# Kernel optimization log

Hardware: AMD Instinct MI355X
Metric: run time of the kernel (lower is better)

## Reference

```python
import jax, jax.numpy as jnp
import numpy as np

NEG_SLOPE = 0.2  # PyG GATConv default LeakyReLU slope
EPS = 1e-16


def gat_conv(x, src, dst, W, att_src, att_dst, bias, concat):
    """One GATConv layer (PyG semantics, self-loops already in src/dst).
    x: [N, Fin]; src/dst: [E'] int; W: [Fin, H*C]; att_*: [H, C]; bias: [H*C] or [C].
    """
    N = x.shape[0]
    H, C = att_src.shape
    h = (x @ W).reshape(N, H, C)                      # [N, H, C]
    a_s = jnp.einsum('nhc,hc->nh', h, att_src)        # [N, H]
    a_d = jnp.einsum('nhc,hc->nh', h, att_dst)        # [N, H]
    logits = jax.nn.leaky_relu(a_s[src] + a_d[dst], NEG_SLOPE)  # [E', H]
    # segment softmax over incoming edges of each destination node
    m = jax.ops.segment_max(logits, dst, num_segments=N)        # [N, H]
    m = jnp.where(jnp.isfinite(m), m, 0.0)
    e = jnp.exp(logits - m[dst])                                # [E', H]
    denom = jax.ops.segment_sum(e, dst, num_segments=N)         # [N, H]
    alpha = e / (denom[dst] + EPS)                              # [E', H]
    msg = h[src] * alpha[:, :, None]                            # [E', H, C]
    out = jax.ops.segment_sum(msg, dst, num_segments=N)         # [N, H, C]
    out = out.reshape(N, H * C) if concat else out.mean(axis=1)
    return out + bias


def setup_inputs() -> dict:
    key = jax.random.key(0)
    ks = jax.random.split(key, 8)
    N, E, IN, HID, OUT, H1 = 50000, 800000, 128, 64, 32, 2
    x = jax.random.normal(ks[0], (N, IN), dtype=jnp.float32)
    edge_index = jax.random.randint(ks[1], (2, E), 0, N, dtype=jnp.int32)
    # glorot-ish scaled params
    W1 = jax.random.normal(ks[2], (IN, H1 * HID), dtype=jnp.float32) * (1.0 / np.sqrt(IN))
    att_src1 = jax.random.normal(ks[3], (H1, HID), dtype=jnp.float32) * (1.0 / np.sqrt(HID))
    att_dst1 = jax.random.normal(ks[4], (H1, HID), dtype=jnp.float32) * (1.0 / np.sqrt(HID))
    bias1 = jnp.zeros((H1 * HID,), dtype=jnp.float32)
    W2 = jax.random.normal(ks[5], (H1 * HID, OUT), dtype=jnp.float32) * (1.0 / np.sqrt(H1 * HID))
    att_src2 = jax.random.normal(ks[6], (1, OUT), dtype=jnp.float32) * (1.0 / np.sqrt(OUT))
    att_dst2 = jax.random.normal(ks[7], (1, OUT), dtype=jnp.float32) * (1.0 / np.sqrt(OUT))
    bias2 = jnp.zeros((OUT,), dtype=jnp.float32)
    return {"x": x, "edge_index": edge_index, "W1": W1, "att_src1": att_src1,
            "att_dst1": att_dst1, "bias1": bias1, "W2": W2, "att_src2": att_src2,
            "att_dst2": att_dst2, "bias2": bias2}


def reference(x, edge_index, W1, att_src1, att_dst1, bias1, W2, att_src2, att_dst2, bias2):
    N = x.shape[0]
    loops = jnp.arange(N, dtype=edge_index.dtype)
    src = jnp.concatenate([edge_index[0], loops])   # add self loops (PyG default)
    dst = jnp.concatenate([edge_index[1], loops])
    h = gat_conv(x, src, dst, W1, att_src1, att_dst1, bias1, concat=True)
    h = jax.nn.relu(h)
    out = gat_conv(h, src, dst, W2, att_src2, att_dst2, bias2, concat=False)
    return out
```

## Files before the change

### kernel.cpp

```cpp
#include <hip/hip_runtime.h>
#include <math.h>


typedef __bf16 bf16x8 __attribute__((ext_vector_type(8)));
typedef float f32x4 __attribute__((ext_vector_type(4)));

__device__ __forceinline__ float lrelu(float x) { return x > 0.f ? x : 0.2f * x; }

__device__ __forceinline__ unsigned short f2bf(float x) {
  unsigned u = __float_as_uint(x);
  return (unsigned short)((u + 0x7fffu + ((u >> 16) & 1u)) >> 16);
}
__device__ __forceinline__ float2 bf2_unpack(unsigned u) {
  return make_float2(__uint_as_float(u << 16), __uint_as_float(u & 0xffff0000u));
}

constexpr int CAP2 = 1408;

union SharedK1 {
  struct { int hist[1024]; int bbase[1024]; } part;
  union { unsigned short bl[32 * 64 * 8]; float accl[64 * 132]; } gem;
};

__launch_bounds__(256)
__global__ void k_csr_gemm1(const int* __restrict__ srcA, const int* __restrict__ dstA,
                            int E, int Nn, int PB, int* __restrict__ gcnt,
                            unsigned* __restrict__ bkt,
                            const float* __restrict__ A, const float* __restrict__ B,
                            unsigned short* __restrict__ Cb,
                            const float* __restrict__ attS, const float* __restrict__ attD,
                            float* __restrict__ asO, float* __restrict__ adO, int M) {
  __shared__ SharedK1 sm;
  const int tid = threadIdx.x;
  if ((int)blockIdx.x < PB) {
    const int NBK = (Nn + 63) >> 6;
    for (int i = tid; i < NBK; i += 256) sm.part.hist[i] = 0;
    __syncthreads();
    const int tot = E + Nn;
    const int g0 = blockIdx.x * 4096;
    unsigned pk[16]; int bk[16], rk[16]; int cnt = 0;
#pragma unroll
    for (int j = 0; j < 16; ++j) {
      int g = g0 + j * 256 + tid;
      if (g >= tot) break;
      int s, d;
      if (g < E) { s = srcA[g]; d = dstA[g]; } else { s = g - E; d = s; }
      int b = d >> 6;
      pk[cnt] = (unsigned)s | ((unsigned)(d & 63) << 16);
      bk[cnt] = b;
      rk[cnt] = atomicAdd(&sm.part.hist[b], 1);
      cnt++;
    }
    __syncthreads();
    for (int i = tid; i < NBK; i += 256) {
      int h = sm.part.hist[i];
      sm.part.bbase[i] = h ? atomicAdd(&gcnt[i], h) : 0;
    }
    __syncthreads();
    for (int j = 0; j < cnt; ++j) {
      int pos = sm.part.bbase[bk[j]] + rk[j];
      if (pos < CAP2) bkt[(size_t)bk[j] * CAP2 + pos] = pk[j];
    }
    return;
  }
  const int lane = tid & 63, w = tid >> 6;
  const int row0 = (blockIdx.x - PB) * 64;
  for (int i = tid; i < 128 * 32; i += 256) {
    int k = i >> 5, n4 = (i & 31) << 2;
    float4 v = *(const float4*)(B + k * 128 + n4);
    int c = k >> 5, q = (k >> 3) & 3, j = k & 7;
    float vv[4] = {v.x, v.y, v.z, v.w};
#pragma unroll
    for (int u2 = 0; u2 < 4; ++u2) {
      int n = n4 + u2, t = n >> 4, l = q * 16 + (n & 15);
      sm.gem.bl[((t * 4 + c) * 64 + l) * 8 + j] = f2bf(vv[u2]);
    }
  }
  int mrow = row0 + 16 * w + (lane & 15);
  bool rok = mrow < M;
  const int q = lane >> 4;
  bf16x8 afr[4];
  union { unsigned short s[8]; bf16x8 b; } cv;
#pragma unroll
  for (int c = 0; c < 4; ++c) {
    float4 u0 = make_float4(0.f, 0.f, 0.f, 0.f), u1 = u0;
    if (rok) {
      const float* ap = A + (size_t)mrow * 128 + c * 32 + q * 8;
      u0 = *(const float4*)ap; u1 = *(const float4*)(ap + 4);
    }
    cv.s[0] = f2bf(u0.x); cv.s[1] = f2bf(u0.y); cv.s[2] = f2bf(u0.z); cv.s[3] = f2bf(u0.w);
    cv.s[4] = f2bf(u1.x); cv.s[5] = f2bf(u1.y); cv.s[6] = f2bf(u1.z); cv.s[7] = f2bf(u1.w);
    afr[c] = cv.b;
  }
  __syncthreads();
  f32x4 acc[8];
#pragma unroll
  for (int t = 0; t < 8; ++t) {
    f32x4 a = {0.f, 0.f, 0.f, 0.f};
#pragma unroll
    for (int c = 0; c < 4; ++c) {
      bf16x8 bf = *(((const bf16x8*)sm.gem.bl) + (t * 4 + c) * 64 + lane);
      a = __builtin_amdgcn_mfma_f32_16x16x32_bf16(afr[c], bf, a, 0, 0, 0);
    }
    acc[t] = a;
  }
  __syncthreads();
  {
    int rbase = 16 * w + q * 4, cl = lane & 15;
#pragma unroll
    for (int t = 0; t < 8; ++t)
#pragma unroll
      for (int r = 0; r < 4; ++r)
        sm.gem.accl[(rbase + r) * 132 + 16 * t + cl] = acc[t][r];
  }
  __syncthreads();
  {
    int row = tid >> 2, cg = tid & 3, c0 = cg * 32;
    int grow = row0 + row;
    const float* ar = &sm.gem.accl[row * 132 + c0];
    float ps = 0.f, pd = 0.f;
    unsigned pkv[16];
#pragma unroll
    for (int u2 = 0; u2 < 8; ++u2) {
      float4 v  = *(const float4*)(ar + u2 * 4);
      float4 s4 = *(const float4*)(attS + c0 + u2 * 4);
      float4 d4 = *(const float4*)(attD + c0 + u2 * 4);
      ps += v.x * s4.x + v.y * s4.y + v.z * s4.z + v.w * s4.w;
      pd += v.x * d4.x + v.y * d4.y + v.z * d4.z + v.w * d4.w;
      pkv[u2 * 2]     = (unsigned)f2bf(v.x) | ((unsigned)f2bf(v.y) << 16);
      pkv[u2 * 2 + 1] = (unsigned)f2bf(v.z) | ((unsigned)f2bf(v.w) << 16);
    }
    ps += __shfl_xor(ps, 1); pd += __shfl_xor(pd, 1);
    if (grow < M) {
      if ((tid & 1) == 0) {
        int head = (tid >> 1) & 1;
        asO[(size_t)grow * 2 + head] = ps; adO[(size_t)grow * 2 + head] = pd;
      }
      unsigned* cp = (unsigned*)(Cb + (size_t)grow * 128 + c0);
      *(uint4*)(cp)      = make_uint4(pkv[0], pkv[1], pkv[2], pkv[3]);
      *(uint4*)(cp + 4)  = make_uint4(pkv[4], pkv[5], pkv[6], pkv[7]);
      *(uint4*)(cp + 8)  = make_uint4(pkv[8], pkv[9], pkv[10], pkv[11]);
      *(uint4*)(cp + 12) = make_uint4(pkv[12], pkv[13], pkv[14], pkv[15]);
    }
  }
}

__launch_bounds__(512)
__global__ void k_fused2(const unsigned* __restrict__ bkt, const int* __restrict__ gcnt,
                         int Nn, int tot,
                         const float* __restrict__ as1, const float* __restrict__ ad1,
                         const float* __restrict__ bias1,
                         const unsigned* __restrict__ h1b,
                         const float* __restrict__ W2,
                         const float* __restrict__ attS, const float* __restrict__ attD,
                         int* __restrict__ offs, unsigned short* __restrict__ csr16,
                         unsigned short* __restrict__ h2b,
                         float* __restrict__ as2, float* __restrict__ ad2) {
  __shared__ unsigned short bl[8 * 64 * 8];
  __shared__ unsigned h2t[64 * 68];
  __shared__ unsigned short srcL[CAP2];
  __shared__ int fc[64], lo[65], cur[64];
  __shared__ float accl[64 * 36];
  __shared__ int baseS;
  const int b = blockIdx.x;
  const int tid = threadIdx.x;
  int m = gcnt[b]; if (m > CAP2) m = CAP2;
  const unsigned* p = bkt + (size_t)b * CAP2;

  for (int i = tid; i < 128 * 8; i += 512) {
    int k = i >> 3, n4 = (i & 7) << 2;
    float4 v = *(const float4*)(W2 + k * 32 + n4);
    int c = k >> 5, q = (k >> 3) & 3, j = k & 7;
    float vv[4] = {v.x, v.y, v.z, v.w};
#pragma unroll
    for (int u2 = 0; u2 < 4; ++u2) {
      int n = n4 + u2, t = n >> 4, l = q * 16 + (n & 15);
      bl[((t * 4 + c) * 64 + l) * 8 + j] = f2bf(vv[u2]);
    }
  }
  if (tid < 64) fc[tid] = 0;
  if (b == 0 && tid == 64) offs[Nn] = tot;
  __syncthreads();
  for (int i = tid; i < m; i += 512) atomicAdd(&fc[p[i] >> 16], 1);
  __syncthreads();
  if (tid < 64) {
    int s = 0;
    for (int c = tid; c < b; c += 64) s += gcnt[c];
#pragma unroll
    for (int o = 32; o; o >>= 1) s += __shfl_xor(s, o);
    if (tid == 0) baseS = s;
    int v = fc[tid], x = v;
#pragma unroll
    for (int o = 1; o < 64; o <<= 1) { int t = __shfl_up(x, o); if (tid >= o) x += t; }
    lo[tid] = x - v;
    cur[tid] = x - v;
    if (tid == 63) lo[64] = x;
  }
  __syncthreads();
  for (int i = tid; i < m; i += 512) {
    unsigned e = p[i];
    int pos = atomicAdd(&cur[e >> 16], 1);
    srcL[pos] = (unsigned short)(e & 0xffffu);
  }
  __syncthreads();
  const int base = baseS;
  for (int i = tid; i < m; i += 512) csr16[base + i] = srcL[i];
  if (tid < 64) {
    int n = (b << 6) + tid;
    if (n < Nn) offs[n] = base + lo[tid];
  }

  const int w = tid >> 6, lane = tid & 63;
  const int head = lane >> 5, el = lane & 31;
  const int pbase = (lane & 32) << 2;
  for (int j8 = 0; j8 < 8; ++j8) {
    int j = w * 8 + j8;
    int n = (b << 6) + j;
    if (n >= Nn) break;
    int beg = lo[j], end = lo[j + 1];
    float2 adn = ((const float2*)ad1)[n];
    float adh = head ? adn.y : adn.x;
    float ax = 0.f, ay = 0.f, den = 0.f;
    int i = beg;
    while (i < end) {
      int mm = end - i; if (mm > 32) mm = 32;
      bool ok = el < mm;
      int sv = ok ? (int)srcL[i + el] : 0;
      float wv = 0.f;
      if (ok) {
        float2 a = ((const float2*)as1)[sv];
        wv = __expf(lrelu((head ? a.y : a.x) + adh));
      }
      int j2 = 0;
      for (; j2 + 4 <= mm; j2 += 4) {
#pragma unroll
        for (int u = 0; u < 4; ++u) {
          int s = __builtin_amdgcn_readlane(sv, j2 + u);
          float ee = __int_as_float(
              __builtin_amdgcn_ds_bpermute(pbase + 4 * (j2 + u), __float_as_int(wv)));
          float2 v = bf2_unpack(h1b[(size_t)s * 64 + lane]);
          ax += ee * v.x; ay += ee * v.y; den += ee;
        }
      }
      for (; j2 < mm; ++j2) {
        int s = __builtin_amdgcn_readlane(sv, j2);
        float ee = __int_as_float(
            __builtin_amdgcn_ds_bpermute(pbase + 4 * j2, __float_as_int(wv)));
        float2 v = bf2_unpack(h1b[(size_t)s * 64 + lane]);
        ax += ee * v.x; ay += ee * v.y; den += ee;
      }
      i += mm;
    }
    float inv = 1.f / (den + 1e-16f);
    const float2 bv = ((const float2*)bias1)[lane];
    float o0 = ax * inv + bv.x; o0 = o0 > 0.f ? o0 : 0.f;
    float o1 = ay * inv + bv.y; o1 = o1 > 0.f ? o1 : 0.f;
    h2t[j * 68 + lane] = (unsigned)f2bf(o0) | ((unsigned)f2bf(o1) << 16);
  }
  __syncthreads();

  {
    int rt = w & 3, ct = w >> 2;
    int mloc = rt * 16 + (lane & 15);
    int q = lane >> 4;
    bf16x8 afr[4];
#pragma unroll
    for (int c = 0; c < 4; ++c) {
      uint4 u = *(const uint4*)&h2t[mloc * 68 + c * 16 + q * 4];
      afr[c] = __builtin_bit_cast(bf16x8, u);
    }
    f32x4 a = {0.f, 0.f, 0.f, 0.f};
#pragma unroll
    for (int c = 0; c < 4; ++c) {
      bf16x8 bf = *(((const bf16x8*)bl) + (ct * 4 + c) * 64 + lane);
      a = __builtin_amdgcn_mfma_f32_16x16x32_bf16(afr[c], bf, a, 0, 0, 0);
    }
    int rbase = rt * 16 + q * 4, cl = lane & 15;
#pragma unroll
    for (int r = 0; r < 4; ++r)
      accl[(rbase + r) * 36 + ct * 16 + cl] = a[r];
  }
  __syncthreads();
  if (tid < 256) {
    int row = tid >> 2, cg = tid & 3, c0 = cg * 8;
    int grow = (b << 6) + row;
    const float* ar = &accl[row * 36 + c0];
    float ps = 0.f, pd = 0.f;
    unsigned pkv[4];
#pragma unroll
    for (int u2 = 0; u2 < 2; ++u2) {
      float4 v  = *(const float4*)(ar + u2 * 4);
      float4 s4 = *(const float4*)(attS + c0 + u2 * 4);
      float4 d4 = *(const float4*)(attD + c0 + u2 * 4);
      ps += v.x * s4.x + v.y * s4.y + v.z * s4.z + v.w * s4.w;
      pd += v.x * d4.x + v.y * d4.y + v.z * d4.z + v.w * d4.w;
      pkv[u2 * 2]     = (unsigned)f2bf(v.x) | ((unsigned)f2bf(v.y) << 16);
      pkv[u2 * 2 + 1] = (unsigned)f2bf(v.z) | ((unsigned)f2bf(v.w) << 16);
    }
    ps += __shfl_xor(ps, 1); ps += __shfl_xor(ps, 2);
    pd += __shfl_xor(pd, 1); pd += __shfl_xor(pd, 2);
    if (grow < Nn) {
      if (cg == 0) { as2[grow] = ps; ad2[grow] = pd; }
      *(uint4*)(h2b + (size_t)grow * 32 + c0) = make_uint4(pkv[0], pkv[1], pkv[2], pkv[3]);
    }
  }
}

__global__ void k_agg2(const unsigned* __restrict__ h2b, const float* __restrict__ as2,
                       const float* __restrict__ ad2, const int* __restrict__ offs,
                       const unsigned short* __restrict__ csr16,
                       const float* __restrict__ bias, float* __restrict__ out, int Nn) {
  int n = blockIdx.x * (blockDim.x >> 6) + (threadIdx.x >> 6);
  if (n >= Nn) return;
  int lane = threadIdx.x & 63;
  int g = lane >> 4, cp = lane & 15;
  int beg = offs[n], end = offs[n + 1];
  float adn = ad2[n];
  float ax = 0.f, ay = 0.f, den = 0.f;
  int i = beg;
  while (i < end) {
    int m = end - i; if (m > 64) m = 64;
    int idx = i + lane;
    bool ok = idx < end;
    int sv = ok ? (int)csr16[idx] : 0;
    float wv = ok ? __expf(lrelu(as2[sv] + adn)) : 0.f;
    for (int j = 0; j < m; j += 4) {
      int jj = j + g;
      float ee = __shfl(wv, jj);
      int s = __shfl(sv, jj);
      float2 v = bf2_unpack(h2b[(size_t)s * 16 + cp]);
      ax += ee * v.x; ay += ee * v.y; den += ee;
    }
    i += m;
  }
  ax += __shfl_xor(ax, 16); ay += __shfl_xor(ay, 16); den += __shfl_xor(den, 16);
  ax += __shfl_xor(ax, 32); ay += __shfl_xor(ay, 32); den += __shfl_xor(den, 32);
  if (lane < 16) {
    float inv = 1.f / (den + 1e-16f);
    const float2 bv = ((const float2*)bias)[cp];
    ((float2*)out)[(size_t)n * 16 + cp] =
        make_float2(ax * inv + bv.x, ay * inv + bv.y);
  }
}

extern "C" void kernel_launch(void* const* d_in, const int* in_sizes, int n_in,
                              void* d_out, int out_size, void* d_ws, size_t ws_size,
                              hipStream_t stream) {
  const float* x      = (const float*)d_in[0];
  const int*   ei     = (const int*)d_in[1];
  const float* W1     = (const float*)d_in[2];
  const float* att_s1 = (const float*)d_in[3];
  const float* att_d1 = (const float*)d_in[4];
  const float* bias1  = (const float*)d_in[5];
  const float* W2     = (const float*)d_in[6];
  const float* att_s2 = (const float*)d_in[7];
  const float* att_d2 = (const float*)d_in[8];
  const float* bias2  = (const float*)d_in[9];
  float* out = (float*)d_out;

  const int N = in_sizes[0] / 128;
  const int E = in_sizes[1] / 2;
  const int* srcA = ei;
  const int* dstA = ei + E;
  const int tot = E + N;
  const int NBK = (N + 63) >> 6;

  char* w = (char*)d_ws;
  auto alloc = [&](size_t bytes) { char* p = w; w += (bytes + 255) / 256 * 256; return p; };
  unsigned short* h1b = (unsigned short*)alloc((size_t)N * 128 * 2);
  unsigned short* h2b = (unsigned short*)alloc((size_t)N * 32 * 2);
  float* as1    = (float*)alloc((size_t)N * 2 * 4);
  float* ad1    = (float*)alloc((size_t)N * 2 * 4);
  float* as2    = (float*)alloc((size_t)N * 4);
  float* ad2    = (float*)alloc((size_t)N * 4);
  int*   gcnt   = (int*)alloc((size_t)NBK * 4);
  unsigned* bkt = (unsigned*)alloc((size_t)NBK * CAP2 * 4);
  int*   offs   = (int*)alloc((size_t)(N + 1) * 4);
  unsigned short* csr16 = (unsigned short*)alloc((size_t)tot * 2);

  hipMemsetAsync(gcnt, 0, (size_t)NBK * 4, stream);

  const int PB = (tot + 4095) / 4096;
  const int GB = (N + 63) / 64;
  k_csr_gemm1<<<PB + GB, 256, 0, stream>>>(srcA, dstA, E, N, PB, gcnt, bkt,
                                           x, W1, h1b, att_s1, att_d1, as1, ad1, N);
  k_fused2<<<NBK, 512, 0, stream>>>(bkt, gcnt, N, tot, as1, ad1, bias1,
                                    (const unsigned*)h1b, W2, att_s2, att_d2,
                                    offs, csr16, h2b, as2, ad2);
  int nb = (N + 3) / 4;
  k_agg2<<<nb, 256, 0, stream>>>((const unsigned*)h2b, as2, ad2, offs, csr16, bias2, out, N);
}
```

Measured before the change: 181.9 us.

## Merge layer-2 aggregation into fused kernel via global spin barrier

k_fused2 now makes each block handle two 64-node buckets, then waits at a grid-wide atomic spin barrier before running the layer-2 aggregation that used to be the separate k_agg2 launch. This removes one kernel launch and its tail gap, and amortises the W2 shared-memory staging over two buckets. The barrier only works if all 391 blocks are resident at once, which launch_bounds(512,4) is meant to help ensure. If they are not co-resident it deadlocks, and halving the block count reduces parallelism in the aggregation phases.

```diff
diff --git a/kernel.cpp b/kernel.cpp
--- a/kernel.cpp
+++ b/kernel.cpp
@@ -145,9 +145,9 @@
   }
 }
 
-__launch_bounds__(512)
+__launch_bounds__(512, 4)
 __global__ void k_fused2(const unsigned* __restrict__ bkt, const int* __restrict__ gcnt,
-                         int Nn, int tot,
+                         int Nn, int tot, int NBK,
                          const float* __restrict__ as1, const float* __restrict__ ad1,
                          const float* __restrict__ bias1,
                          const unsigned* __restrict__ h1b,
@@ -155,17 +155,17 @@
                          const float* __restrict__ attS, const float* __restrict__ attD,
                          int* __restrict__ offs, unsigned short* __restrict__ csr16,
                          unsigned short* __restrict__ h2b,
-                         float* __restrict__ as2, float* __restrict__ ad2) {
+                         float* __restrict__ as2, float* __restrict__ ad2,
+                         const float* __restrict__ bias2, float* __restrict__ out,
+                         unsigned* __restrict__ barrier_ctr) {
   __shared__ unsigned short bl[8 * 64 * 8];
   __shared__ unsigned h2t[64 * 68];
   __shared__ unsigned short srcL[CAP2];
   __shared__ int fc[64], lo[65], cur[64];
   __shared__ float accl[64 * 36];
   __shared__ int baseS;
-  const int b = blockIdx.x;
   const int tid = threadIdx.x;
-  int m = gcnt[b]; if (m > CAP2) m = CAP2;
-  const unsigned* p = bkt + (size_t)b * CAP2;
+  const int w = tid >> 6, lane = tid & 63;
 
   for (int i = tid; i < 128 * 8; i += 512) {
     int k = i >> 3, n4 = (i & 7) << 2;
@@ -178,168 +178,183 @@
       bl[((t * 4 + c) * 64 + l) * 8 + j] = f2bf(vv[u2]);
     }
   }
-  if (tid < 64) fc[tid] = 0;
-  if (b == 0 && tid == 64) offs[Nn] = tot;
-  __syncthreads();
-  for (int i = tid; i < m; i += 512) atomicAdd(&fc[p[i] >> 16], 1);
-  __syncthreads();
-  if (tid < 64) {
-    int s = 0;
-    for (int c = tid; c < b; c += 64) s += gcnt[c];
-#pragma unroll
-    for (int o = 32; o; o >>= 1) s += __shfl_xor(s, o);
-    if (tid == 0) baseS = s;
-    int v = fc[tid], x = v;
-#pragma unroll
-    for (int o = 1; o < 64; o <<= 1) { int t = __shfl_up(x, o); if (tid >= o) x += t; }
-    lo[tid] = x - v;
-    cur[tid] = x - v;
-    if (tid == 63) lo[64] = x;
-  }
-  __syncthreads();
-  for (int i = tid; i < m; i += 512) {
-    unsigned e = p[i];
-    int pos = atomicAdd(&cur[e >> 16], 1);
-    srcL[pos] = (unsigned short)(e & 0xffffu);
-  }
-  __syncthreads();
-  const int base = baseS;
-  for (int i = tid; i < m; i += 512) csr16[base + i] = srcL[i];
-  if (tid < 64) {
-    int n = (b << 6) + tid;
-    if (n < Nn) offs[n] = base + lo[tid];
-  }
-
-  const int w = tid >> 6, lane = tid & 63;
-  const int head = lane >> 5, el = lane & 31;
-  const int pbase = (lane & 32) << 2;
-  for (int j8 = 0; j8 < 8; ++j8) {
-    int j = w * 8 + j8;
-    int n = (b << 6) + j;
-    if (n >= Nn) break;
-    int beg = lo[j], end = lo[j + 1];
-    float2 adn = ((const float2*)ad1)[n];
-    float adh = head ? adn.y : adn.x;
-    float ax = 0.f, ay = 0.f, den = 0.f;
-    int i = beg;
-    while (i < end) {
-      int mm = end - i; if (mm > 32) mm = 32;
-      bool ok = el < mm;
-      int sv = ok ? (int)srcL[i + el] : 0;
-      float wv = 0.f;
-      if (ok) {
-        float2 a = ((const float2*)as1)[sv];
-        wv = __expf(lrelu((head ? a.y : a.x) + adh));
-      }
-      int j2 = 0;
-      for (; j2 + 4 <= mm; j2 += 4) {
-#pragma unroll
-        for (int u = 0; u < 4; ++u) {
-          int s = __builtin_amdgcn_readlane(sv, j2 + u);
+  if (blockIdx.x == 0 && tid == 0) offs[Nn] = tot;
+
+  for (int half = 0; half < 2; ++half) {
+    const int b = blockIdx.x * 2 + half;
+    if (b >= NBK) break;
+    int m = gcnt[b]; if (m > CAP2) m = CAP2;
+    const unsigned* p = bkt + (size_t)b * CAP2;
+    if (tid < 64) fc[tid] = 0;
+    __syncthreads();
+    for (int i = tid; i < m; i += 512) atomicAdd(&fc[p[i] >> 16], 1);
+    __syncthreads();
+    if (tid < 64) {
+      int s = 0;
+      for (int c = tid; c < b; c += 64) s += gcnt[c];
+#pragma unroll
+      for (int o = 32; o; o >>= 1) s += __shfl_xor(s, o);
+      if (tid == 0) baseS = s;
+      int v = fc[tid], x = v;
+#pragma unroll
+      for (int o = 1; o < 64; o <<= 1) { int t = __shfl_up(x, o); if (tid >= o) x += t; }
+      lo[tid] = x - v;
+      cur[tid] = x - v;
+      if (tid == 63) lo[64] = x;
+    }
+    __syncthreads();
+    for (int i = tid; i < m; i += 512) {
+      unsigned e = p[i];
+      int pos = atomicAdd(&cur[e >> 16], 1);
+      srcL[pos] = (unsigned short)(e & 0xffffu);
+    }
+    __syncthreads();
+    const int base = baseS;
+    for (int i = tid; i < m; i += 512) csr16[base + i] = srcL[i];
+    if (tid < 64) {
+      int n = (b << 6) + tid;
+      if (n < Nn) offs[n] = base + lo[tid];
+    }
+
+    const int head = lane >> 5, el = lane & 31;
+    const int pbase = (lane & 32) << 2;
+    for (int j8 = 0; j8 < 8; ++j8) {
+      int j = w * 8 + j8;
+      int n = (b << 6) + j;
+      if (n >= Nn) break;
+      int beg = lo[j], end = lo[j + 1];
+      float2 adn = ((const float2*)ad1)[n];
+      float adh = head ? adn.y : adn.x;
+      float ax = 0.f, ay = 0.f, den = 0.f;
+      int i = beg;
+      while (i < end) {
+        int mm = end - i; if (mm > 32) mm = 32;
+        bool ok = el < mm;
+        int sv = ok ? (int)srcL[i + el] : 0;
+        float wv = 0.f;
+        if (ok) {
+          float2 a = ((const float2*)as1)[sv];
+          wv = __expf(lrelu((head ? a.y : a.x) + adh));
+        }
+        int j2 = 0;
+        for (; j2 + 4 <= mm; j2 += 4) {
+#pragma unroll
+          for (int u = 0; u < 4; ++u) {
+            int s = __builtin_amdgcn_readlane(sv, j2 + u);
+            float ee = __int_as_float(
+                __builtin_amdgcn_ds_bpermute(pbase + 4 * (j2 + u), __float_as_int(wv)));
+            float2 v = bf2_unpack(h1b[(size_t)s * 64 + lane]);
+            ax += ee * v.x; ay += ee * v.y; den += ee;
+          }
+        }
+        for (; j2 < mm; ++j2) {
+          int s = __builtin_amdgcn_readlane(sv, j2);
           float ee = __int_as_float(
-              __builtin_amdgcn_ds_bpermute(pbase + 4 * (j2 + u), __float_as_int(wv)));
+              __builtin_amdgcn_ds_bpermute(pbase + 4 * j2, __float_as_int(wv)));
           float2 v = bf2_unpack(h1b[(size_t)s * 64 + lane]);
           ax += ee * v.x; ay += ee * v.y; den += ee;
         }
-      }
-      for (; j2 < mm; ++j2) {
-        int s = __builtin_amdgcn_readlane(sv, j2);
-        float ee = __int_as_float(
-            __builtin_amdgcn_ds_bpermute(pbase + 4 * j2, __float_as_int(wv)));
-        float2 v = bf2_unpack(h1b[(size_t)s * 64 + lane]);
-        ax += ee * v.x; ay += ee * v.y; den += ee;
-      }
-      i += mm;
-    }
-    float inv = 1.f / (den + 1e-16f);
-    const float2 bv = ((const float2*)bias1)[lane];
-    float o0 = ax * inv + bv.x; o0 = o0 > 0.f ? o0 : 0.f;
-    float o1 = ay * inv + bv.y; o1 = o1 > 0.f ? o1 : 0.f;
-    h2t[j * 68 + lane] = (unsigned)f2bf(o0) | ((unsigned)f2bf(o1) << 16);
+        i += mm;
+      }
+      float inv = 1.f / (den + 1e-16f);
+      const float2 bv = ((const float2*)bias1)[lane];
+      float o0 = ax * inv + bv.x; o0 = o0 > 0.f ? o0 : 0.f;
+      float o1 = ay * inv + bv.y; o1 = o1 > 0.f ? o1 : 0.f;
+      h2t[j * 68 + lane] = (unsigned)f2bf(o0) | ((unsigned)f2bf(o1) << 16);
+    }
+    __syncthreads();
+
+    {
+      int rt = w & 3, ct = w >> 2;
+      int mloc = rt * 16 + (lane & 15);
+      int q = lane >> 4;
+      bf16x8 afr[4];
+#pragma unroll
+      for (int c = 0; c < 4; ++c) {
+        uint4 u = *(const uint4*)&h2t[mloc * 68 + c * 16 + q * 4];
+        afr[c] = __builtin_bit_cast(bf16x8, u);
+      }
+      f32x4 a = {0.f, 0.f, 0.f, 0.f};
+#pragma unroll
+      for (int c = 0; c < 4; ++c) {
+        bf16x8 bf = *(((const bf16x8*)bl) + (ct * 4 + c) * 64 + lane);
+        a = __builtin_amdgcn_mfma_f32_16x16x32_bf16(afr[c], bf, a, 0, 0, 0);
+      }
+      int rbase = rt * 16 + q * 4, cl = lane & 15;
+#pragma unroll
+      for (int r = 0; r < 4; ++r)
+        accl[(rbase + r) * 36 + ct * 16 + cl] = a[r];
+    }
+    __syncthreads();
+    if (tid < 256) {
+      int row = tid >> 2, cg = tid & 3, c0 = cg * 8;
+      int grow = (b << 6) + row;
+      const float* ar = &accl[row * 36 + c0];
+      float ps = 0.f, pd = 0.f;
+      unsigned pkv[4];
+#pragma unroll
+      for (int u2 = 0; u2 < 2; ++u2) {
+        float4 v  = *(const float4*)(ar + u2 * 4);
+        float4 s4 = *(const float4*)(attS + c0 + u2 * 4);
+        float4 d4 = *(const float4*)(attD + c0 + u2 * 4);
+        ps += v.x * s4.x + v.y * s4.y + v.z * s4.z + v.w * s4.w;
+        pd += v.x * d4.x + v.y * d4.y + v.z * d4.z + v.w * d4.w;
+        pkv[u2 * 2]     = (unsigned)f2bf(v.x) | ((unsigned)f2bf(v.y) << 16);
+        pkv[u2 * 2 + 1] = (unsigned)f2bf(v.z) | ((unsigned)f2bf(v.w) << 16);
+      }
+      ps += __shfl_xor(ps, 1); ps += __shfl_xor(ps, 2);
+      pd += __shfl_xor(pd, 1); pd += __shfl_xor(pd, 2);
+      if (grow < Nn) {
+        if (cg == 0) { as2[grow] = ps; ad2[grow] = pd; }
+        *(uint4*)(h2b + (size_t)grow * 32 + c0) = make_uint4(pkv[0], pkv[1], pkv[2], pkv[3]);
+      }
+    }
+    __syncthreads();
+  }
+
+  if (tid == 0) {
+    __threadfence();
+    atomicAdd(barrier_ctr, 1u);
+    while (__hip_atomic_load(barrier_ctr, __ATOMIC_ACQUIRE, __HIP_MEMORY_SCOPE_AGENT)
+           < (unsigned)gridDim.x)
+      __builtin_amdgcn_s_sleep(16);
+    __threadfence();
   }
   __syncthreads();
 
   {
-    int rt = w & 3, ct = w >> 2;
-    int mloc = rt * 16 + (lane & 15);
-    int q = lane >> 4;
-    bf16x8 afr[4];
-#pragma unroll
-    for (int c = 0; c < 4; ++c) {
-      uint4 u = *(const uint4*)&h2t[mloc * 68 + c * 16 + q * 4];
-      afr[c] = __builtin_bit_cast(bf16x8, u);
-    }
-    f32x4 a = {0.f, 0.f, 0.f, 0.f};
-#pragma unroll
-    for (int c = 0; c < 4; ++c) {
-      bf16x8 bf = *(((const bf16x8*)bl) + (ct * 4 + c) * 64 + lane);
-      a = __builtin_amdgcn_mfma_f32_16x16x32_bf16(afr[c], bf, a, 0, 0, 0);
-    }
-    int rbase = rt * 16 + q * 4, cl = lane & 15;
-#pragma unroll
-    for (int r = 0; r < 4; ++r)
-      accl[(rbase + r) * 36 + ct * 16 + cl] = a[r];
-  }
-  __syncthreads();
-  if (tid < 256) {
-    int row = tid >> 2, cg = tid & 3, c0 = cg * 8;
-    int grow = (b << 6) + row;
-    const float* ar = &accl[row * 36 + c0];
-    float ps = 0.f, pd = 0.f;
-    unsigned pkv[4];
-#pragma unroll
-    for (int u2 = 0; u2 < 2; ++u2) {
-      float4 v  = *(const float4*)(ar + u2 * 4);
-      float4 s4 = *(const float4*)(attS + c0 + u2 * 4);
-      float4 d4 = *(const float4*)(attD + c0 + u2 * 4);
-      ps += v.x * s4.x + v.y * s4.y + v.z * s4.z + v.w * s4.w;
-      pd += v.x * d4.x + v.y * d4.y + v.z * d4.z + v.w * d4.w;
-      pkv[u2 * 2]     = (unsigned)f2bf(v.x) | ((unsigned)f2bf(v.y) << 16);
-      pkv[u2 * 2 + 1] = (unsigned)f2bf(v.z) | ((unsigned)f2bf(v.w) << 16);
-    }
-    ps += __shfl_xor(ps, 1); ps += __shfl_xor(ps, 2);
-    pd += __shfl_xor(pd, 1); pd += __shfl_xor(pd, 2);
-    if (grow < Nn) {
-      if (cg == 0) { as2[grow] = ps; ad2[grow] = pd; }
-      *(uint4*)(h2b + (size_t)grow * 32 + c0) = make_uint4(pkv[0], pkv[1], pkv[2], pkv[3]);
-    }
-  }
-}
-
-__global__ void k_agg2(const unsigned* __restrict__ h2b, const float* __restrict__ as2,
-                       const float* __restrict__ ad2, const int* __restrict__ offs,
-                       const unsigned short* __restrict__ csr16,
-                       const float* __restrict__ bias, float* __restrict__ out, int Nn) {
-  int n = blockIdx.x * (blockDim.x >> 6) + (threadIdx.x >> 6);
-  if (n >= Nn) return;
-  int lane = threadIdx.x & 63;
-  int g = lane >> 4, cp = lane & 15;
-  int beg = offs[n], end = offs[n + 1];
-  float adn = ad2[n];
-  float ax = 0.f, ay = 0.f, den = 0.f;
-  int i = beg;
-  while (i < end) {
-    int m = end - i; if (m > 64) m = 64;
-    int idx = i + lane;
-    bool ok = idx < end;
-    int sv = ok ? (int)csr16[idx] : 0;
-    float wv = ok ? __expf(lrelu(as2[sv] + adn)) : 0.f;
-    for (int j = 0; j < m; j += 4) {
-      int jj = j + g;
-      float ee = __shfl(wv, jj);
-      int s = __shfl(sv, jj);
-      float2 v = bf2_unpack(h2b[(size_t)s * 16 + cp]);
-      ax += ee * v.x; ay += ee * v.y; den += ee;
-    }
-    i += m;
-  }
-  ax += __shfl_xor(ax, 16); ay += __shfl_xor(ay, 16); den += __shfl_xor(den, 16);
-  ax += __shfl_xor(ax, 32); ay += __shfl_xor(ay, 32); den += __shfl_xor(den, 32);
-  if (lane < 16) {
-    float inv = 1.f / (den + 1e-16f);
-    const float2 bv = ((const float2*)bias)[cp];
-    ((float2*)out)[(size_t)n * 16 + cp] =
-        make_float2(ax * inv + bv.x, ay * inv + bv.y);
+    const int g = lane >> 4, cp = lane & 15;
+    for (int t = 0; t < 16; ++t) {
+      int n = blockIdx.x * 128 + w * 16 + t;
+      if (n >= Nn) break;
+      int beg = offs[n], end = offs[n + 1];
+      float adn = ad2[n];
+      float ax = 0.f, ay = 0.f, den = 0.f;
+      int i = beg;
+      while (i < end) {
+        int m = end - i; if (m > 64) m = 64;
+        int idx = i + lane;
+        bool ok = idx < end;
+        int sv = ok ? (int)csr16[idx] : 0;
+        float wv = ok ? __expf(lrelu(as2[sv] + adn)) : 0.f;
+        for (int j = 0; j < m; j += 4) {
+          int jj = j + g;
+          float ee = __shfl(wv, jj);
+          int s = __shfl(sv, jj);
+          float2 v = bf2_unpack(((const unsigned*)h2b)[(size_t)s * 16 + cp]);
+          ax += ee * v.x; ay += ee * v.y; den += ee;
+        }
+        i += m;
+      }
+      ax += __shfl_xor(ax, 16); ay += __shfl_xor(ay, 16); den += __shfl_xor(den, 16);
+      ax += __shfl_xor(ax, 32); ay += __shfl_xor(ay, 32); den += __shfl_xor(den, 32);
+      if (lane < 16) {
+        float inv = 1.f / (den + 1e-16f);
+        const float2 bv = ((const float2*)bias2)[cp];
+        ((float2*)out)[(size_t)n * 16 + cp] =
+            make_float2(ax * inv + bv.x, ay * inv + bv.y);
+      }
+    }
   }
 }
 
@@ -374,19 +389,20 @@
   float* as2    = (float*)alloc((size_t)N * 4);
   float* ad2    = (float*)alloc((size_t)N * 4);
   int*   gcnt   = (int*)alloc((size_t)NBK * 4);
+  unsigned* bctr= (unsigned*)alloc(4);
   unsigned* bkt = (unsigned*)alloc((size_t)NBK * CAP2 * 4);
   int*   offs   = (int*)alloc((size_t)(N + 1) * 4);
   unsigned short* csr16 = (unsigned short*)alloc((size_t)tot * 2);
 
   hipMemsetAsync(gcnt, 0, (size_t)NBK * 4, stream);
+  hipMemsetAsync(bctr, 0, 4, stream);
 
   const int PB = (tot + 4095) / 4096;
   const int GB = (N + 63) / 64;
   k_csr_gemm1<<<PB + GB, 256, 0, stream>>>(srcA, dstA, E, N, PB, gcnt, bkt,
                                            x, W1, h1b, att_s1, att_d1, as1, ad1, N);
-  k_fused2<<<NBK, 512, 0, stream>>>(bkt, gcnt, N, tot, as1, ad1, bias1,
+  const int K2B = (NBK + 1) / 2;
+  k_fused2<<<K2B, 512, 0, stream>>>(bkt, gcnt, N, tot, NBK, as1, ad1, bias1,
                                     (const unsigned*)h1b, W2, att_s2, att_d2,
-                                    offs, csr16, h2b, as2, ad2);
-  int nb = (N + 3) / 4;
-  k_agg2<<<nb, 256, 0, stream>>>((const unsigned*)h2b, as2, ad2, offs, csr16, bias2, out, N);
+                                    offs, csr16, h2b, as2, ad2, bias2, out, bctr);
 }
```

Measured after the change: 301.6 us. 1.66x slower.

## Widen per-lane gathers to 8 bytes and process multiple edges per wave in aggregations

Applied to the files above, without the earlier changes.

Both layer-1 and layer-2 aggregation loops now have each lane load a uint2 (4 bf16 features) instead of one 32-bit word. The lanes are split into groups that handle different edges at the same time, and the partial sums are combined with cross-lane xor shuffles at the end. In layer 1 a wave now covers two edges per step with half-row gathers, and the inner loop is unrolled so eight gathers are in flight. The aim is fewer, wider memory transactions and more memory-level parallelism. The cost is extra bpermute traffic, a final reduction, and more register pressure.

```diff
diff --git a/kernel.cpp b/kernel.cpp
--- a/kernel.cpp
+++ b/kernel.cpp
@@ -211,51 +211,73 @@
   }
 
   const int w = tid >> 6, lane = tid & 63;
-  const int head = lane >> 5, el = lane & 31;
-  const int pbase = (lane & 32) << 2;
+  const int c2 = lane & 31, e2 = lane >> 5;
+  const int wb = (c2 >> 4) << 7;
+  const uint2* h1u2 = (const uint2*)h1b;
   for (int j8 = 0; j8 < 8; ++j8) {
     int j = w * 8 + j8;
     int n = (b << 6) + j;
     if (n >= Nn) break;
     int beg = lo[j], end = lo[j + 1];
     float2 adn = ((const float2*)ad1)[n];
-    float adh = head ? adn.y : adn.x;
-    float ax = 0.f, ay = 0.f, den = 0.f;
+    float adh = (lane & 32) ? adn.y : adn.x;
+    float ax0 = 0.f, ax1 = 0.f, ax2 = 0.f, ax3 = 0.f, den = 0.f;
     int i = beg;
     while (i < end) {
       int mm = end - i; if (mm > 32) mm = 32;
+      int el = lane & 31;
       bool ok = el < mm;
       int sv = ok ? (int)srcL[i + el] : 0;
       float wv = 0.f;
       if (ok) {
         float2 a = ((const float2*)as1)[sv];
-        wv = __expf(lrelu((head ? a.y : a.x) + adh));
+        wv = __expf(lrelu(((lane & 32) ? a.y : a.x) + adh));
       }
       int j2 = 0;
-      for (; j2 + 4 <= mm; j2 += 4) {
-#pragma unroll
-        for (int u = 0; u < 4; ++u) {
-          int s = __builtin_amdgcn_readlane(sv, j2 + u);
-          float ee = __int_as_float(
-              __builtin_amdgcn_ds_bpermute(pbase + 4 * (j2 + u), __float_as_int(wv)));
-          float2 v = bf2_unpack(h1b[(size_t)s * 64 + lane]);
-          ax += ee * v.x; ay += ee * v.y; den += ee;
+      for (; j2 + 16 <= mm; j2 += 16) {
+        float ee[8]; uint2 vv[8];
+#pragma unroll
+        for (int u = 0; u < 8; ++u) {
+          int k = j2 + 2 * u + e2;
+          ee[u] = __int_as_float(__builtin_amdgcn_ds_bpermute(wb + 4 * k, __float_as_int(wv)));
+          int s = __builtin_amdgcn_ds_bpermute(4 * k, sv);
+          vv[u] = h1u2[(size_t)s * 32 + c2];
+        }
+#pragma unroll
+        for (int u = 0; u < 8; ++u) {
+          float2 p0 = bf2_unpack(vv[u].x), p1 = bf2_unpack(vv[u].y);
+          ax0 += ee[u] * p0.x; ax1 += ee[u] * p0.y;
+          ax2 += ee[u] * p1.x; ax3 += ee[u] * p1.y;
+          den += ee[u];
         }
       }
-      for (; j2 < mm; ++j2) {
-        int s = __builtin_amdgcn_readlane(sv, j2);
-        float ee = __int_as_float(
-            __builtin_amdgcn_ds_bpermute(pbase + 4 * j2, __float_as_int(wv)));
-        float2 v = bf2_unpack(h1b[(size_t)s * 64 + lane]);
-        ax += ee * v.x; ay += ee * v.y; den += ee;
+      for (; j2 < mm; j2 += 2) {
+        int k = j2 + e2;
+        float ee = __int_as_float(__builtin_amdgcn_ds_bpermute(wb + 4 * k, __float_as_int(wv)));
+        int s = __builtin_amdgcn_ds_bpermute(4 * k, sv);
+        uint2 v = h1u2[(size_t)s * 32 + c2];
+        float2 p0 = bf2_unpack(v.x), p1 = bf2_unpack(v.y);
+        ax0 += ee * p0.x; ax1 += ee * p0.y;
+        ax2 += ee * p1.x; ax3 += ee * p1.y;
+        den += ee;
       }
       i += mm;
     }
-    float inv = 1.f / (den + 1e-16f);
-    const float2 bv = ((const float2*)bias1)[lane];
-    float o0 = ax * inv + bv.x; o0 = o0 > 0.f ? o0 : 0.f;
-    float o1 = ay * inv + bv.y; o1 = o1 > 0.f ? o1 : 0.f;
-    h2t[j * 68 + lane] = (unsigned)f2bf(o0) | ((unsigned)f2bf(o1) << 16);
+    ax0 += __shfl_xor(ax0, 32); ax1 += __shfl_xor(ax1, 32);
+    ax2 += __shfl_xor(ax2, 32); ax3 += __shfl_xor(ax3, 32);
+    den += __shfl_xor(den, 32);
+    if (lane < 32) {
+      float inv = 1.f / (den + 1e-16f);
+      const float4 bv = *(const float4*)(bias1 + 4 * c2);
+      float o0 = ax0 * inv + bv.x; o0 = o0 > 0.f ? o0 : 0.f;
+      float o1 = ax1 * inv + bv.y; o1 = o1 > 0.f ? o1 : 0.f;
+      float o2 = ax2 * inv + bv.z; o2 = o2 > 0.f ? o2 : 0.f;
+      float o3 = ax3 * inv + bv.w; o3 = o3 > 0.f ? o3 : 0.f;
+      uint2 pk;
+      pk.x = (unsigned)f2bf(o0) | ((unsigned)f2bf(o1) << 16);
+      pk.y = (unsigned)f2bf(o2) | ((unsigned)f2bf(o3) << 16);
+      *(uint2*)&h2t[j * 68 + 2 * c2] = pk;
+    }
   }
   __syncthreads();
 
@@ -306,17 +328,17 @@
   }
 }
 
-__global__ void k_agg2(const unsigned* __restrict__ h2b, const float* __restrict__ as2,
+__global__ void k_agg2(const uint2* __restrict__ h2u2, const float* __restrict__ as2,
                        const float* __restrict__ ad2, const int* __restrict__ offs,
                        const unsigned short* __restrict__ csr16,
                        const float* __restrict__ bias, float* __restrict__ out, int Nn) {
   int n = blockIdx.x * (blockDim.x >> 6) + (threadIdx.x >> 6);
   if (n >= Nn) return;
   int lane = threadIdx.x & 63;
-  int g = lane >> 4, cp = lane & 15;
+  int g8 = lane >> 3, c2 = lane & 7;
   int beg = offs[n], end = offs[n + 1];
   float adn = ad2[n];
-  float ax = 0.f, ay = 0.f, den = 0.f;
+  float ax0 = 0.f, ax1 = 0.f, ax2 = 0.f, ax3 = 0.f, den = 0.f;
   int i = beg;
   while (i < end) {
     int m = end - i; if (m > 64) m = 64;
@@ -324,22 +346,43 @@
     bool ok = idx < end;
     int sv = ok ? (int)csr16[idx] : 0;
     float wv = ok ? __expf(lrelu(as2[sv] + adn)) : 0.f;
-    for (int j = 0; j < m; j += 4) {
-      int jj = j + g;
-      float ee = __shfl(wv, jj);
-      int s = __shfl(sv, jj);
-      float2 v = bf2_unpack(h2b[(size_t)s * 16 + cp]);
-      ax += ee * v.x; ay += ee * v.y; den += ee;
+    int j = 0;
+    for (; j + 16 <= m; j += 16) {
+      int k0 = j + g8, k1 = j + 8 + g8;
+      float e0 = __shfl(wv, k0); int s0 = __shfl(sv, k0);
+      float e1 = __shfl(wv, k1); int s1 = __shfl(sv, k1);
+      uint2 v0 = h2u2[(size_t)s0 * 8 + c2];
+      uint2 v1 = h2u2[(size_t)s1 * 8 + c2];
+      float2 a0 = bf2_unpack(v0.x), b0 = bf2_unpack(v0.y);
+      float2 a1 = bf2_unpack(v1.x), b1 = bf2_unpack(v1.y);
+      ax0 += e0 * a0.x + e1 * a1.x; ax1 += e0 * a0.y + e1 * a1.y;
+      ax2 += e0 * b0.x + e1 * b1.x; ax3 += e0 * b0.y + e1 * b1.y;
+      den += e0 + e1;
+    }
+    for (; j < m; j += 8) {
+      int k = j + g8;
+      float ee = __shfl(wv, k);
+      int s = __shfl(sv, k);
+      uint2 v = h2u2[(size_t)s * 8 + c2];
+      float2 p0 = bf2_unpack(v.x), p1 = bf2_unpack(v.y);
+      ax0 += ee * p0.x; ax1 += ee * p0.y;
+      ax2 += ee * p1.x; ax3 += ee * p1.y;
+      den += ee;
     }
     i += m;
   }
-  ax += __shfl_xor(ax, 16); ay += __shfl_xor(ay, 16); den += __shfl_xor(den, 16);
-  ax += __shfl_xor(ax, 32); ay += __shfl_xor(ay, 32); den += __shfl_xor(den, 32);
-  if (lane < 16) {
+#pragma unroll
+  for (int o = 8; o < 64; o <<= 1) {
+    ax0 += __shfl_xor(ax0, o); ax1 += __shfl_xor(ax1, o);
+    ax2 += __shfl_xor(ax2, o); ax3 += __shfl_xor(ax3, o);
+    den += __shfl_xor(den, o);
+  }
+  if (lane < 8) {
     float inv = 1.f / (den + 1e-16f);
-    const float2 bv = ((const float2*)bias)[cp];
-    ((float2*)out)[(size_t)n * 16 + cp] =
-        make_float2(ax * inv + bv.x, ay * inv + bv.y);
+    const float4 bv = *(const float4*)(bias + 4 * c2);
+    *(float4*)(out + (size_t)n * 32 + 4 * c2) =
+        make_float4(ax0 * inv + bv.x, ax1 * inv + bv.y,
+                    ax2 * inv + bv.z, ax3 * inv + bv.w);
   }
 }
 
@@ -388,5 +431,5 @@
                                     (const unsigned*)h1b, W2, att_s2, att_d2,
                                     offs, csr16, h2b, as2, ad2);
   int nb = (N + 3) / 4;
-  k_agg2<<<nb, 256, 0, stream>>>((const unsigned*)h2b, as2, ad2, offs, csr16, bias2, out, N);
-}
+  k_agg2<<<nb, 256, 0, stream>>>((const uint2*)h2b, as2, ad2, offs, csr16, bias2, out, N);
+}
```

Result: slower. 205.0 us (+12.7%).
